# Kernel optimization log

Measured on AMD Instinct MI355X. Metric: run time of the kernel, lower is better.

## Reference

```python
import jax, jax.numpy as jnp
import numpy as np

K = 4096          # infeatures
N = 4096          # outfeatures (already multiple of 32, padding = 0)
M = 8192
GROUPS = 32       # K / group_size, group_size = 128


def setup_inputs() -> dict:
    key = jax.random.key(0)
    k1, k2, k3, k4, k5, k6 = jax.random.split(key, 6)
    x = jax.random.normal(k1, (M, K), dtype=jnp.float16)
    # packed INT4 weights: 8 nibbles per int32 along the K dimension
    q_weight = jax.random.randint(k2, (K // 8, N), 0, 2**31 - 1, dtype=jnp.int32)
    # packed 4-bit group scales: 8 nibbles per int32 along the N dimension
    q_scale = jax.random.randint(k3, (GROUPS, N // 8), 0, 2**31 - 1, dtype=jnp.int32)
    q_scale_max = (jax.random.uniform(k4, (GROUPS,), dtype=jnp.float32) + 0.5).astype(jnp.float16)
    q_invperm = jax.random.permutation(k5, K).astype(jnp.int32)
    bias = (jax.random.normal(k6, (N,), dtype=jnp.float32) * 0.02).astype(jnp.float16)
    return {"x": x, "q_weight": q_weight, "q_scale": q_scale,
            "q_scale_max": q_scale_max, "q_invperm": q_invperm, "bias": bias}


def _unpack_nibbles(packed, axis):
    # packed int32 -> 8 unsigned 4-bit values expanded along `axis`
    shifts = jnp.arange(8, dtype=jnp.int32) * 4
    shp = [1] * (packed.ndim + 1)
    shp[axis + 1] = 8
    vals = (jnp.expand_dims(packed, axis + 1) >> shifts.reshape(shp)) & 0xF
    out_shape = list(packed.shape)
    out_shape[axis] *= 8
    return vals.reshape(out_shape)


def reference(x, q_weight, q_scale, q_scale_max, q_invperm, bias):
    # --- group-wise INT4 dequantization (EXL2-style scale math) ---
    # per-group/column scale: ((s4 + 1)^2) * (q_scale_max / 256)
    s4 = _unpack_nibbles(q_scale, axis=1).astype(jnp.float16)          # [G, N]
    smax = (q_scale_max.astype(jnp.float32) / 256.0).astype(jnp.float16)
    scale = (s4 + 1.0) * (s4 + 1.0) * smax[:, None]                    # [G, N]
    w4 = _unpack_nibbles(q_weight, axis=0)                              # [K, N], 0..15
    group_size = w4.shape[0] // scale.shape[0]
    scale_rows = jnp.repeat(scale, group_size, axis=0)                  # [K, N]
    W = (w4.astype(jnp.float16) - jnp.float16(8.0)) * scale_rows        # [K, N] fp16
    # --- row permutation fused with GEMM: x is gathered by q_perm ---
    q_perm = jnp.argsort(q_invperm)                                     # [K]
    xp = jnp.take(x.astype(jnp.float16), q_perm, axis=1)                # [M, K]
    out = jnp.matmul(xp, W, preferred_element_type=jnp.float32).astype(jnp.float16)
    out = out + bias
    return out.astype(x.dtype)
```

## Files before the change

### kernel.cpp

```cpp
#include <hip/hip_runtime.h>
#include <stdint.h>

#define K_DIM 4096
#define N_DIM 4096
#define M_DIM 8192

#define BM 256
#define BN 128
#define BK 64
#define NT (K_DIM / BK)

typedef __bf16 bf16x8 __attribute__((ext_vector_type(8)));
typedef _Float16 f16x8 __attribute__((ext_vector_type(8)));
typedef unsigned short u16x8 __attribute__((ext_vector_type(8)));
typedef float floatx4 __attribute__((ext_vector_type(4)));

__device__ __attribute__((aligned(256))) unsigned short g_Bt[(size_t)N_DIM * K_DIM];
__device__ __attribute__((aligned(256))) unsigned short g_X [(size_t)M_DIM * K_DIM];
__device__ int g_flags[2];

__device__ __forceinline__ void global_to_lds16(const void* g, void* l) {
    __builtin_amdgcn_global_load_lds(
        (const __attribute__((address_space(1))) uint32_t*)g,
        (__attribute__((address_space(3))) uint32_t*)l,
        16, 0, 0);
}

#define LDS_FENCE() asm volatile("" ::: "memory")

__global__ void probe_kernel(const void* xraw, const int* candA, const int* candB) {
    __shared__ int s_insane, s_small, s_badA, s_badB;
    if (threadIdx.x == 0) { s_insane = 0; s_small = 0; s_badA = 0; s_badB = 0; }
    __syncthreads();
    const uint16_t* xw = (const uint16_t*)xraw;
    int insane = 0, small = 0;
    for (int i = threadIdx.x; i < 8192; i += 256) {
        uint16_t a = (uint16_t)(xw[2 * i] & 0x7FFF);
        if (a >= 0x4300) insane++;
        if (a > 0 && a < 0x3000) small++;
    }
    int badA = 0, badB = 0;
    for (int i = threadIdx.x; i < 4096; i += 256) {
        if ((unsigned)candA[i] >= 4096u) badA++;
        if ((unsigned)candB[i] >= 4096u) badB++;
    }
    atomicAdd(&s_insane, insane); atomicAdd(&s_small, small);
    atomicAdd(&s_badA, badA);     atomicAdd(&s_badB, badB);
    __syncthreads();
    if (threadIdx.x == 0) {
        int mode = 0;
        if (s_insane > 32) mode = 1;
        else if (s_small > 100) mode = 2;
        g_flags[0] = mode;
        g_flags[1] = (s_badA > 0 && s_badB == 0) ? 1 : 0;
    }
}

__global__ void __launch_bounds__(256) convert_x_kernel(const void* xraw) {
    if (g_flags[0] != 1) return;
    const size_t nchunk = (size_t)M_DIM * K_DIM / 8;
    const float* xf = (const float*)xraw;
    for (size_t c = (size_t)blockIdx.x * 256 + threadIdx.x; c < nchunk;
         c += (size_t)gridDim.x * 256) {
        size_t base = c * 8;
        float4 v0 = *(const float4*)(xf + base);
        float4 v1 = *(const float4*)(xf + base + 4);
        u16x8 o;
        _Float16 h;
        h = (_Float16)v0.x; o[0] = __builtin_bit_cast(unsigned short, h);
        h = (_Float16)v0.y; o[1] = __builtin_bit_cast(unsigned short, h);
        h = (_Float16)v0.z; o[2] = __builtin_bit_cast(unsigned short, h);
        h = (_Float16)v0.w; o[3] = __builtin_bit_cast(unsigned short, h);
        h = (_Float16)v1.x; o[4] = __builtin_bit_cast(unsigned short, h);
        h = (_Float16)v1.y; o[5] = __builtin_bit_cast(unsigned short, h);
        h = (_Float16)v1.z; o[6] = __builtin_bit_cast(unsigned short, h);
        h = (_Float16)v1.w; o[7] = __builtin_bit_cast(unsigned short, h);
        *(u16x8*)(g_X + base) = o;
    }
}

__global__ void __launch_bounds__(256) dequant_perm_kernel(
    const int* __restrict__ q_weight,
    const int* __restrict__ q_scale,
    const void* __restrict__ qsm_raw,
    const int* __restrict__ candA, const int* __restrict__ candB)
{
    __shared__ __attribute__((aligned(16))) unsigned short lds[16 * 136];

    const int mode = g_flags[0];
    const int* q_invperm = g_flags[1] ? candB : candA;

    const int n_l  = threadIdx.x & 15;
    const int jp_l = threadIdx.x >> 4;
    const int n  = blockIdx.x * 16 + n_l;
    const int j0 = (blockIdx.y * 16 + jp_l) << 3;

    int4 ip0 = *(const int4*)(q_invperm + j0);
    int4 ip1 = *(const int4*)(q_invperm + j0 + 4);
    int ks[8] = {ip0.x, ip0.y, ip0.z, ip0.w, ip1.x, ip1.y, ip1.z, ip1.w};

    const int nshift = (n & 7) << 2;
    const int scol = n >> 3;

    u16x8 ov;
#pragma unroll
    for (int u = 0; u < 8; ++u) {
        int k = ks[u] & (K_DIM - 1);
        int w4 = (q_weight[(size_t)(k >> 3) * N_DIM + n] >> ((k & 7) << 2)) & 0xF;
        int g = k >> 7;
        int s4 = (q_scale[g * (N_DIM / 8) + scol] >> nshift) & 0xF;
        float smax;
        if (mode == 1)      smax = ((const float*)qsm_raw)[g];
        else if (mode == 2) smax = (float)((const _Float16*)qsm_raw)[g];
        else                smax = (float)((const __bf16*)qsm_raw)[g];
        float sp1 = (float)(s4 + 1);
        float w = (float)(w4 - 8) * (sp1 * sp1 * smax * (1.0f / 256.0f));
        if (mode != 0) { _Float16 h = (_Float16)w; ov[u] = __builtin_bit_cast(unsigned short, h); }
        else           { __bf16   b = (__bf16)w;   ov[u] = __builtin_bit_cast(unsigned short, b); }
    }
    *(u16x8*)&lds[n_l * 136 + jp_l * 8] = ov;
    __syncthreads();

    const int row = threadIdx.x >> 4;
    const int c16 = threadIdx.x & 15;
    u16x8 t = *(const u16x8*)&lds[row * 136 + c16 * 8];
    *(u16x8*)(g_Bt + (size_t)(blockIdx.x * 16 + row) * K_DIM
              + (size_t)blockIdx.y * 128 + c16 * 8) = t;
}

template <bool F16>
__global__ void __launch_bounds__(512, 2) gemm_bt_kernel(
    const void* __restrict__ xraw,
    const void* __restrict__ bias_candA, const void* __restrict__ bias_candB,
    void* __restrict__ outraw)
{
    const int mode = g_flags[0];
    if (F16 != (mode != 0)) return;

    __shared__ __attribute__((aligned(128))) unsigned short sm[3 * BM * BK + 3 * BN * BK];
    const int SB = 3 * BM * BK;

    const void* bias_raw = g_flags[1] ? bias_candA : bias_candB;
    const unsigned short* __restrict__ Xp =
        (mode == 1) ? g_X : (const unsigned short*)xraw;
    const unsigned short* __restrict__ Bt = g_Bt;

    const int tid  = threadIdx.x;
    const int wave = tid >> 6;
    const int lane = tid & 63;

    const int orig = blockIdx.y * 32 + blockIdx.x;
    const int swz  = (orig & 7) * (1024 >> 3) + (orig >> 3);
    const int bn0  = (swz & 31) * BN;
    const int bm0  = (swz >> 5) * BM;

    const int lrow8 = lane >> 3;
    const int ksw   = ((lane & 7) ^ lrow8) << 3;
    const size_t aoff = (size_t)(bm0 + wave * 32 + lrow8) * K_DIM + ksw;
    const size_t boff = (size_t)(bn0 + wave * 16 + lrow8) * K_DIM + ksw;
    const int aldsb = (wave * 4) * 512;
    const int bldsb = (wave * 2) * 512;

    const int wm   = (wave >> 1) << 6;
    const int wn   = (wave & 1) << 6;
    const int frow = lane & 15;
    const int fk   = (lane >> 4) << 3;
    const int ksw8 = (lane & 7) << 3;

    floatx4 acc[4][4] = {};

#pragma unroll
    for (int tt = 0; tt < 2; ++tt) {
#pragma unroll
        for (int c = 0; c < 4; ++c)
            global_to_lds16(Xp + aoff + (size_t)c * (8 * K_DIM) + tt * BK,
                            &sm[tt * (BM * BK) + aldsb + c * 512]);
#pragma unroll
        for (int c = 0; c < 2; ++c)
            global_to_lds16(Bt + boff + (size_t)c * (8 * K_DIM) + tt * BK,
                            &sm[SB + tt * (BN * BK) + bldsb + c * 512]);
    }
    asm volatile("s_waitcnt vmcnt(6)" ::: "memory");
    LDS_FENCE();
    __builtin_amdgcn_s_barrier();
    LDS_FENCE();

    int cur = 0;
#pragma unroll 1
    for (int t = 0; t < NT; ++t) {
        int nb = cur + 2; if (nb >= 3) nb -= 3;
        const int curA = cur * (BM * BK);
        const int curB = SB + cur * (BN * BK);
        const bool stage = (t + 2 < NT);
        const int kt2 = (t + 2) * BK;

#pragma unroll
        for (int ks = 0; ks < 2; ++ks) {
            u16x8 a[4], b[4];
            const int kb = (ks * 32 + fk) ^ ksw8;
#pragma unroll
            for (int i = 0; i < 4; ++i)
                a[i] = *(const u16x8*)&sm[curA + (wm + i * 16 + frow) * 64 + kb];
#pragma unroll
            for (int j = 0; j < 4; ++j)
                b[j] = *(const u16x8*)&sm[curB + (wn + j * 16 + frow) * 64 + kb];

            if (stage) {
                if (ks == 0) {
#pragma unroll
                    for (int c = 0; c < 3; ++c)
                        global_to_lds16(Xp + aoff + (size_t)c * (8 * K_DIM) + kt2,
                                        &sm[nb * (BM * BK) + aldsb + c * 512]);
                } else {
                    global_to_lds16(Xp + aoff + (size_t)3 * (8 * K_DIM) + kt2,
                                    &sm[nb * (BM * BK) + aldsb + 3 * 512]);
#pragma unroll
                    for (int c = 0; c < 2; ++c)
                        global_to_lds16(Bt + boff + (size_t)c * (8 * K_DIM) + kt2,
                                        &sm[SB + nb * (BN * BK) + bldsb + c * 512]);
                }
            }
            if (ks == 1) {
                if (stage) asm volatile("s_waitcnt vmcnt(6)" ::: "memory");
                else       asm volatile("s_waitcnt vmcnt(0)" ::: "memory");
            }
            LDS_FENCE();
            __builtin_amdgcn_s_barrier();
            LDS_FENCE();

            __builtin_amdgcn_s_setprio(1);
#pragma unroll
            for (int i = 0; i < 4; ++i)
#pragma unroll
                for (int j = 0; j < 4; ++j) {
                    if constexpr (F16)
                        acc[i][j] = __builtin_amdgcn_mfma_f32_16x16x32_f16(
                            __builtin_bit_cast(f16x8, a[i]),
                            __builtin_bit_cast(f16x8, b[j]), acc[i][j], 0, 0, 0);
                    else
                        acc[i][j] = __builtin_amdgcn_mfma_f32_16x16x32_bf16(
                            __builtin_bit_cast(bf16x8, a[i]),
                            __builtin_bit_cast(bf16x8, b[j]), acc[i][j], 0, 0, 0);
                }
            __builtin_amdgcn_s_setprio(0);

            LDS_FENCE();
            __builtin_amdgcn_s_barrier();
            LDS_FENCE();
        }
        cur = cur + 1; if (cur >= 3) cur = 0;
    }

    const int ccol = lane & 15;
    const int crow = (lane >> 4) << 2;
#pragma unroll
    for (int j = 0; j < 4; ++j) {
        const int col = bn0 + wn + j * 16 + ccol;
        float bv;
        if (mode == 1)      bv = ((const float*)bias_raw)[col];
        else if (mode == 2) bv = (float)((const _Float16*)bias_raw)[col];
        else                bv = (float)((const __bf16*)bias_raw)[col];
#pragma unroll
        for (int i = 0; i < 4; ++i) {
            const int row = bm0 + wm + i * 16 + crow;
#pragma unroll
            for (int r = 0; r < 4; ++r) {
                float v = acc[i][j][r] + bv;
                size_t idx = (size_t)(row + r) * N_DIM + col;
                if (mode == 1)      ((float*)outraw)[idx] = v;
                else if (mode == 2) ((_Float16*)outraw)[idx] = (_Float16)v;
                else                ((__bf16*)outraw)[idx] = (__bf16)v;
            }
        }
    }
}

extern "C" void kernel_launch(void* const* d_in, const int* in_sizes, int n_in,
                              void* d_out, int out_size, void* d_ws, size_t ws_size,
                              hipStream_t stream) {
    int idx_x = 0, idx_qw = 1, idx_qs = 2, idx_qsm = 3, idx_a = -1, idx_b = -1;
    for (int i = 0; i < n_in; ++i) {
        switch (in_sizes[i]) {
            case 33554432: idx_x = i; break;
            case 2097152:  idx_qw = i; break;
            case 16384:    idx_qs = i; break;
            case 32:       idx_qsm = i; break;
            case 4096:     (idx_a < 0 ? idx_a : idx_b) = i; break;
            default: break;
        }
    }
    if (idx_a < 0) idx_a = 4;
    if (idx_b < 0) idx_b = 5;

    const void* xraw  = d_in[idx_x];
    const int*  qw    = (const int*)d_in[idx_qw];
    const int*  qs    = (const int*)d_in[idx_qs];
    const void* qsm   = d_in[idx_qsm];
    const int*  candA = (const int*)d_in[idx_a];
    const int*  candB = (const int*)d_in[idx_b];

    probe_kernel<<<1, 256, 0, stream>>>(xraw, candA, candB);
    convert_x_kernel<<<2048, 256, 0, stream>>>(xraw);
    dim3 dqg(N_DIM / 16, (K_DIM / 8) / 16);
    dequant_perm_kernel<<<dqg, 256, 0, stream>>>(qw, qs, qsm, candA, candB);
    dim3 grid(N_DIM / BN, M_DIM / BM);
    gemm_bt_kernel<true ><<<grid, 512, 0, stream>>>(xraw, d_in[idx_a], d_in[idx_b], d_out);
    gemm_bt_kernel<false><<<grid, 512, 0, stream>>>(xraw, d_in[idx_a], d_in[idx_b], d_out);
}
```

Before: 547.7 us.

## Enlarge GEMM tile to 256x256 with double-buffered four-phase schedule

Grows the GEMM block tile from 256x128 to 256x256, giving each wave a 128x64 accumulator footprint. The old triple-buffered LDS pipeline becomes a double-buffered one in which each K step is split into four MFMA phases, with global-to-LDS loads for the next tile interleaved between them. The aim is to raise arithmetic intensity and cut global and LDS traffic per FLOP. The cost is more register pressure from 32 accumulators, which may hurt occupancy, plus more barriers per iteration. It also spreads the input probe across 32 blocks and adds a finalize kernel to reduce the counts.

```diff
diff --git a/kernel.cpp b/kernel.cpp
--- a/kernel.cpp
+++ b/kernel.cpp
@@ -6,7 +6,7 @@
 #define M_DIM 8192
 
 #define BM 256
-#define BN 128
+#define BN 256
 #define BK 64
 #define NT (K_DIM / BK)
 
@@ -18,6 +18,7 @@
 __device__ __attribute__((aligned(256))) unsigned short g_Bt[(size_t)N_DIM * K_DIM];
 __device__ __attribute__((aligned(256))) unsigned short g_X [(size_t)M_DIM * K_DIM];
 __device__ int g_flags[2];
+__device__ int g_counts[4];
 
 __device__ __forceinline__ void global_to_lds16(const void* g, void* l) {
     __builtin_amdgcn_global_load_lds(
@@ -27,33 +28,40 @@
 }
 
 #define LDS_FENCE() asm volatile("" ::: "memory")
+#define BARRIER() do { LDS_FENCE(); __builtin_amdgcn_s_barrier(); LDS_FENCE(); } while (0)
 
 __global__ void probe_kernel(const void* xraw, const int* candA, const int* candB) {
-    __shared__ int s_insane, s_small, s_badA, s_badB;
-    if (threadIdx.x == 0) { s_insane = 0; s_small = 0; s_badA = 0; s_badB = 0; }
+    __shared__ int s[4];
+    if (threadIdx.x < 4) s[threadIdx.x] = 0;
     __syncthreads();
     const uint16_t* xw = (const uint16_t*)xraw;
+    const int gidx = blockIdx.x * 256 + threadIdx.x;
     int insane = 0, small = 0;
-    for (int i = threadIdx.x; i < 8192; i += 256) {
-        uint16_t a = (uint16_t)(xw[2 * i] & 0x7FFF);
+    {
+        uint16_t a = (uint16_t)(xw[2 * gidx] & 0x7FFF);
         if (a >= 0x4300) insane++;
         if (a > 0 && a < 0x3000) small++;
     }
     int badA = 0, badB = 0;
-    for (int i = threadIdx.x; i < 4096; i += 256) {
-        if ((unsigned)candA[i] >= 4096u) badA++;
-        if ((unsigned)candB[i] >= 4096u) badB++;
-    }
-    atomicAdd(&s_insane, insane); atomicAdd(&s_small, small);
-    atomicAdd(&s_badA, badA);     atomicAdd(&s_badB, badB);
+    if (gidx < 4096) {
+        if ((unsigned)candA[gidx] >= 4096u) badA++;
+        if ((unsigned)candB[gidx] >= 4096u) badB++;
+    }
+    atomicAdd(&s[0], insane); atomicAdd(&s[1], small);
+    atomicAdd(&s[2], badA);   atomicAdd(&s[3], badB);
     __syncthreads();
-    if (threadIdx.x == 0) {
-        int mode = 0;
-        if (s_insane > 32) mode = 1;
-        else if (s_small > 100) mode = 2;
-        g_flags[0] = mode;
-        g_flags[1] = (s_badA > 0 && s_badB == 0) ? 1 : 0;
-    }
+    if (threadIdx.x < 4 && s[threadIdx.x] != 0) atomicAdd(&g_counts[threadIdx.x], s[threadIdx.x]);
+}
+
+__global__ void finalize_kernel() {
+    int insane = g_counts[0], small = g_counts[1];
+    int badA = g_counts[2], badB = g_counts[3];
+    int mode = 0;
+    if (insane > 32) mode = 1;
+    else if (small > 100) mode = 2;
+    g_flags[0] = mode;
+    g_flags[1] = (badA > 0 && badB == 0) ? 1 : 0;
+    g_counts[0] = g_counts[1] = g_counts[2] = g_counts[3] = 0;
 }
 
 __global__ void __launch_bounds__(256) convert_x_kernel(const void* xraw) {
@@ -137,8 +145,9 @@
     const int mode = g_flags[0];
     if (F16 != (mode != 0)) return;
 
-    __shared__ __attribute__((aligned(128))) unsigned short sm[3 * BM * BK + 3 * BN * BK];
-    const int SB = 3 * BM * BK;
+    __shared__ __attribute__((aligned(128))) unsigned short sm[4 * 256 * 64];
+    const int ASZ = 256 * 64;
+    const int SB  = 2 * ASZ;
 
     const void* bias_raw = g_flags[1] ? bias_candA : bias_candB;
     const unsigned short* __restrict__ Xp =
@@ -149,120 +158,136 @@
     const int wave = tid >> 6;
     const int lane = tid & 63;
 
-    const int orig = blockIdx.y * 32 + blockIdx.x;
-    const int swz  = (orig & 7) * (1024 >> 3) + (orig >> 3);
-    const int bn0  = (swz & 31) * BN;
-    const int bm0  = (swz >> 5) * BM;
+    const int orig = blockIdx.y * 16 + blockIdx.x;
+    const int swz  = (orig & 7) * 64 + (orig >> 3);
+    const int bn0  = (swz & 15) * BN;
+    const int bm0  = (swz >> 4) * BM;
 
     const int lrow8 = lane >> 3;
     const int ksw   = ((lane & 7) ^ lrow8) << 3;
-    const size_t aoff = (size_t)(bm0 + wave * 32 + lrow8) * K_DIM + ksw;
-    const size_t boff = (size_t)(bn0 + wave * 16 + lrow8) * K_DIM + ksw;
-    const int aldsb = (wave * 4) * 512;
-    const int bldsb = (wave * 2) * 512;
-
-    const int wm   = (wave >> 1) << 6;
-    const int wn   = (wave & 1) << 6;
-    const int frow = lane & 15;
-    const int fk   = (lane >> 4) << 3;
-    const int ksw8 = (lane & 7) << 3;
-
-    floatx4 acc[4][4] = {};
-
-#pragma unroll
-    for (int tt = 0; tt < 2; ++tt) {
-#pragma unroll
-        for (int c = 0; c < 4; ++c)
-            global_to_lds16(Xp + aoff + (size_t)c * (8 * K_DIM) + tt * BK,
-                            &sm[tt * (BM * BK) + aldsb + c * 512]);
-#pragma unroll
-        for (int c = 0; c < 2; ++c)
-            global_to_lds16(Bt + boff + (size_t)c * (8 * K_DIM) + tt * BK,
-                            &sm[SB + tt * (BN * BK) + bldsb + c * 512]);
-    }
-    asm volatile("s_waitcnt vmcnt(6)" ::: "memory");
-    LDS_FENCE();
-    __builtin_amdgcn_s_barrier();
-    LDS_FENCE();
+    const size_t aoff = (size_t)(bm0 + wave * 8 + lrow8) * K_DIM + ksw;
+    const size_t boff = (size_t)(bn0 + wave * 8 + lrow8) * K_DIM + ksw;
+    const int ldsw = (wave * 8) * 64;
+
+    const int w_m16 = (wave >> 2) << 4;
+    const int w_n16 = (wave & 3) << 4;
+    const int frow  = lane & 15;
+    const int fk    = (lane >> 4) << 3;
+    const int ksw8  = (lane & 7) << 3;
+
+    floatx4 acc[8][4] = {};
+    u16x8 a[4][2], b[4][2];
+
+#define STAGE_A(bufbase, h, c, ktt) \
+    global_to_lds16(Xp + aoff + (size_t)((h) * 128 + (c) * 64) * K_DIM + (ktt), \
+                    &sm[(bufbase) + ((h) * 128 + (c) * 64) * 64 + ldsw])
+#define STAGE_B(bufbase, h, c, ktt) \
+    global_to_lds16(Bt + boff + (size_t)((h) * 128 + (c) * 64) * K_DIM + (ktt), \
+                    &sm[SB + (bufbase) + ((h) * 128 + (c) * 64) * 64 + ldsw])
+
+#define MFMA_PH(ibase, jbase) do { \
+    __builtin_amdgcn_s_setprio(1); \
+    _Pragma("unroll") \
+    for (int ii = 0; ii < 4; ++ii) \
+        _Pragma("unroll") \
+        for (int jj = 0; jj < 2; ++jj) \
+            _Pragma("unroll") \
+            for (int kh = 0; kh < 2; ++kh) { \
+                if constexpr (F16) \
+                    acc[(ibase) + ii][(jbase) + jj] = __builtin_amdgcn_mfma_f32_16x16x32_f16( \
+                        __builtin_bit_cast(f16x8, a[ii][kh]), \
+                        __builtin_bit_cast(f16x8, b[(jbase) + jj][kh]), \
+                        acc[(ibase) + ii][(jbase) + jj], 0, 0, 0); \
+                else \
+                    acc[(ibase) + ii][(jbase) + jj] = __builtin_amdgcn_mfma_f32_16x16x32_bf16( \
+                        __builtin_bit_cast(bf16x8, a[ii][kh]), \
+                        __builtin_bit_cast(bf16x8, b[(jbase) + jj][kh]), \
+                        acc[(ibase) + ii][(jbase) + jj], 0, 0, 0); \
+            } \
+    __builtin_amdgcn_s_setprio(0); \
+} while (0)
+
+    STAGE_A(0, 0, 0, 0); STAGE_A(0, 0, 1, 0);
+    STAGE_B(0, 0, 0, 0); STAGE_B(0, 0, 1, 0);
+    STAGE_B(0, 1, 0, 0); STAGE_B(0, 1, 1, 0);
+    STAGE_A(0, 1, 0, 0); STAGE_A(0, 1, 1, 0);
+    asm volatile("s_waitcnt vmcnt(4)" ::: "memory");
+    BARRIER();
 
     int cur = 0;
 #pragma unroll 1
     for (int t = 0; t < NT; ++t) {
-        int nb = cur + 2; if (nb >= 3) nb -= 3;
-        const int curA = cur * (BM * BK);
-        const int curB = SB + cur * (BN * BK);
-        const bool stage = (t + 2 < NT);
-        const int kt2 = (t + 2) * BK;
-
-#pragma unroll
-        for (int ks = 0; ks < 2; ++ks) {
-            u16x8 a[4], b[4];
-            const int kb = (ks * 32 + fk) ^ ksw8;
-#pragma unroll
-            for (int i = 0; i < 4; ++i)
-                a[i] = *(const u16x8*)&sm[curA + (wm + i * 16 + frow) * 64 + kb];
-#pragma unroll
-            for (int j = 0; j < 4; ++j)
-                b[j] = *(const u16x8*)&sm[curB + (wn + j * 16 + frow) * 64 + kb];
-
-            if (stage) {
-                if (ks == 0) {
-#pragma unroll
-                    for (int c = 0; c < 3; ++c)
-                        global_to_lds16(Xp + aoff + (size_t)c * (8 * K_DIM) + kt2,
-                                        &sm[nb * (BM * BK) + aldsb + c * 512]);
-                } else {
-                    global_to_lds16(Xp + aoff + (size_t)3 * (8 * K_DIM) + kt2,
-                                    &sm[nb * (BM * BK) + aldsb + 3 * 512]);
-#pragma unroll
-                    for (int c = 0; c < 2; ++c)
-                        global_to_lds16(Bt + boff + (size_t)c * (8 * K_DIM) + kt2,
-                                        &sm[SB + nb * (BN * BK) + bldsb + c * 512]);
-                }
-            }
-            if (ks == 1) {
-                if (stage) asm volatile("s_waitcnt vmcnt(6)" ::: "memory");
-                else       asm volatile("s_waitcnt vmcnt(0)" ::: "memory");
-            }
-            LDS_FENCE();
-            __builtin_amdgcn_s_barrier();
-            LDS_FENCE();
-
-            __builtin_amdgcn_s_setprio(1);
-#pragma unroll
-            for (int i = 0; i < 4; ++i)
-#pragma unroll
-                for (int j = 0; j < 4; ++j) {
-                    if constexpr (F16)
-                        acc[i][j] = __builtin_amdgcn_mfma_f32_16x16x32_f16(
-                            __builtin_bit_cast(f16x8, a[i]),
-                            __builtin_bit_cast(f16x8, b[j]), acc[i][j], 0, 0, 0);
-                    else
-                        acc[i][j] = __builtin_amdgcn_mfma_f32_16x16x32_bf16(
-                            __builtin_bit_cast(bf16x8, a[i]),
-                            __builtin_bit_cast(bf16x8, b[j]), acc[i][j], 0, 0, 0);
-                }
-            __builtin_amdgcn_s_setprio(0);
-
-            LDS_FENCE();
-            __builtin_amdgcn_s_barrier();
-            LDS_FENCE();
+        const int nxt = cur ^ 1;
+        const int curA = cur * ASZ;
+        const int curB = cur * ASZ;
+        const int nbA = nxt * ASZ;
+        const int nbB = nxt * ASZ;
+        const bool st = (t + 1 < NT);
+        const int kt1 = (t + 1) * BK;
+
+#pragma unroll
+        for (int ii = 0; ii < 4; ++ii)
+#pragma unroll
+            for (int kh = 0; kh < 2; ++kh)
+                a[ii][kh] = *(const u16x8*)&sm[curA + (ii * 32 + w_m16 + frow) * 64
+                                              + ((kh * 32 + fk) ^ ksw8)];
+#pragma unroll
+        for (int j = 0; j < 2; ++j)
+#pragma unroll
+            for (int kh = 0; kh < 2; ++kh)
+                b[j][kh] = *(const u16x8*)&sm[SB + curB + (j * 64 + w_n16 + frow) * 64
+                                              + ((kh * 32 + fk) ^ ksw8)];
+        if (st) { STAGE_A(nbA, 0, 0, kt1); STAGE_A(nbA, 0, 1, kt1); }
+        if (st) asm volatile("s_waitcnt vmcnt(4) lgkmcnt(0)" ::: "memory");
+        else    asm volatile("s_waitcnt vmcnt(2) lgkmcnt(0)" ::: "memory");
+        BARRIER();
+        MFMA_PH(0, 0);
+
+#pragma unroll
+        for (int j = 2; j < 4; ++j)
+#pragma unroll
+            for (int kh = 0; kh < 2; ++kh)
+                b[j][kh] = *(const u16x8*)&sm[SB + curB + (j * 64 + w_n16 + frow) * 64
+                                              + ((kh * 32 + fk) ^ ksw8)];
+        if (st) { STAGE_B(nbB, 0, 0, kt1); STAGE_B(nbB, 0, 1, kt1); }
+        if (st) asm volatile("s_waitcnt vmcnt(4) lgkmcnt(0)" ::: "memory");
+        else    asm volatile("s_waitcnt vmcnt(0) lgkmcnt(0)" ::: "memory");
+        BARRIER();
+        MFMA_PH(0, 2);
+
+#pragma unroll
+        for (int ii = 0; ii < 4; ++ii)
+#pragma unroll
+            for (int kh = 0; kh < 2; ++kh)
+                a[ii][kh] = *(const u16x8*)&sm[curA + ((ii + 4) * 32 + w_m16 + frow) * 64
+                                               + ((kh * 32 + fk) ^ ksw8)];
+        if (st) { STAGE_B(nbB, 1, 0, kt1); STAGE_B(nbB, 1, 1, kt1); }
+        asm volatile("s_waitcnt lgkmcnt(0)" ::: "memory");
+        BARRIER();
+        MFMA_PH(4, 2);
+
+        if (st) {
+            STAGE_A(nbA, 1, 0, kt1); STAGE_A(nbA, 1, 1, kt1);
+            asm volatile("s_waitcnt vmcnt(4)" ::: "memory");
         }
-        cur = cur + 1; if (cur >= 3) cur = 0;
+        BARRIER();
+        MFMA_PH(4, 0);
+
+        cur = nxt;
     }
 
     const int ccol = lane & 15;
     const int crow = (lane >> 4) << 2;
 #pragma unroll
     for (int j = 0; j < 4; ++j) {
-        const int col = bn0 + wn + j * 16 + ccol;
+        const int col = bn0 + j * 64 + w_n16 + ccol;
         float bv;
         if (mode == 1)      bv = ((const float*)bias_raw)[col];
         else if (mode == 2) bv = (float)((const _Float16*)bias_raw)[col];
         else                bv = (float)((const __bf16*)bias_raw)[col];
 #pragma unroll
-        for (int i = 0; i < 4; ++i) {
-            const int row = bm0 + wm + i * 16 + crow;
+        for (int i = 0; i < 8; ++i) {
+            const int row = bm0 + i * 32 + w_m16 + crow;
 #pragma unroll
             for (int r = 0; r < 4; ++r) {
                 float v = acc[i][j][r] + bv;
@@ -273,6 +298,9 @@
             }
         }
     }
+#undef STAGE_A
+#undef STAGE_B
+#undef MFMA_PH
 }
 
 extern "C" void kernel_launch(void* const* d_in, const int* in_sizes, int n_in,
@@ -299,7 +327,8 @@
     const int*  candA = (const int*)d_in[idx_a];
     const int*  candB = (const int*)d_in[idx_b];
 
-    probe_kernel<<<1, 256, 0, stream>>>(xraw, candA, candB);
+    probe_kernel<<<32, 256, 0, stream>>>(xraw, candA, candB);
+    finalize_kernel<<<1, 1, 0, stream>>>();
     convert_x_kernel<<<2048, 256, 0, stream>>>(xraw);
     dim3 dqg(N_DIM / 16, (K_DIM / 8) / 16);
     dequant_perm_kernel<<<dqg, 256, 0, stream>>>(qw, qs, qsm, candA, candB);
```

Measured after the change: 479.9 us. -12.4%, faster.
